# Performance work log

Measured on AMD Instinct MI355X. Metric: run time of the kernel, lower is better.

## Reference

```python
import jax, jax.numpy as jnp
import numpy as np

EPS = 1e-06        # normalize eps and log eps (module's self.eps)
PDIST_EPS = 1e-06  # torch.nn.PairwiseDistance default eps: ||x1 - x2 + eps||_2

A, C, F = 4096, 8, 64


def setup_inputs() -> dict:
    key = jax.random.key(0)
    x = jax.random.normal(key, (A, C, F), dtype=jnp.float32)
    return {"x": x}


def reference(x) -> jnp.ndarray:
    a = x.shape[0]
    c = x.shape[1]
    # F.normalize(p=2, dim=-1, eps=EPS): x / max(||x||_2, eps)
    nrm = jnp.linalg.norm(x, axis=-1, keepdims=True)
    xn = x / jnp.maximum(nrm, EPS)
    # pairwise cosine similarity per group: [C, A, A]
    sim = jnp.einsum('acf,bcf->cab', xn, xn)
    # mask self-similarity on the diagonal with -1
    diag = jnp.eye(a, dtype=bool)[None, :, :]
    sim = jnp.where(diag, -1.0, sim)
    # nearest neighbor per (c, a): argmax over b -> [C, A] -> [A, C]
    idx = jnp.argmax(sim, axis=-1).T
    # gather matched embeddings: x_match[a, c, f] = xn[idx[a, c], c, f]
    x_match = xn[idx, jnp.arange(c)[None, :], :]
    # PairwiseDistance(p=2, eps=1e-6): ||x - x_match + eps||_2 over last dim
    min_dist = jnp.linalg.norm(xn - x_match + PDIST_EPS, axis=-1)
    loss = -jnp.mean(jnp.log(min_dist + EPS))
    return loss
```

## Files before the change

kernel.cpp:

```cpp
#include <hip/hip_runtime.h>
#include <math.h>

#define AN 4096
#define CN 8
#define FN 64
#define ACN (AN*CN)

typedef __attribute__((ext_vector_type(8))) short bf16x8;
typedef __attribute__((ext_vector_type(4))) float f32x4;

__device__ inline unsigned short f2bf(float f) {
    unsigned u = __float_as_uint(f);
    unsigned r = ((u >> 16) & 1) + 0x7FFFu;
    return (unsigned short)((u + r) >> 16);
}

__global__ __launch_bounds__(256) void k1_normalize(const float* __restrict__ x,
                                                    float* __restrict__ xn,
                                                    unsigned short* __restrict__ xnb)
{
    int tid  = threadIdx.x;
    int grp  = tid >> 4;
    int slot = tid & 15;
    int V = blockIdx.x * 16 + grp;
    const float4 v = *(const float4*)(x + (size_t)V * FN + slot * 4);
    float ss = v.x*v.x + v.y*v.y + v.z*v.z + v.w*v.w;
    ss += __shfl_xor(ss, 1);
    ss += __shfl_xor(ss, 2);
    ss += __shfl_xor(ss, 4);
    ss += __shfl_xor(ss, 8);
    float sc = 1.0f / fmaxf(sqrtf(ss), 1e-6f);
    float4 o; o.x = v.x*sc; o.y = v.y*sc; o.z = v.z*sc; o.w = v.w*sc;
    *(float4*)(xn + (size_t)V * FN + slot * 4) = o;
    int a = V >> 3, c = V & 7;
    ushort4 ob;
    ob.x = f2bf(o.x); ob.y = f2bf(o.y); ob.z = f2bf(o.z); ob.w = f2bf(o.w);
    *(ushort4*)(xnb + ((size_t)c * AN + a) * FN + slot * 4) = ob;
}

__global__ __launch_bounds__(256, 2) void k2_argmax(const unsigned short* __restrict__ xnb,
                                                    unsigned int* __restrict__ pP)
{
    __shared__ uint4 lds4[3 * 1024];

    int blk  = blockIdx.x;
    int half = blk & 1;
    int rt   = (blk >> 1) & 31;
    int c    = blk >> 6;
    int a0   = rt * 128;
    int b0base = half * 2048;

    const uint4* __restrict__ Xc4 = (const uint4*)(xnb + (size_t)c * AN * FN);

    int tid  = threadIdx.x;
    int lane = tid & 63;
    int w    = tid >> 6;
    int wr   = w >> 1;
    int wc   = w & 1;
    int l15  = lane & 15;
    int quad = lane >> 4;

    int srow   = tid >> 3;
    int schunk = tid & 7;

    #pragma unroll
    for (int s = 0; s < 4; ++s) {
        int r = srow + 32 * s;
        lds4[r * 8 + (schunk ^ (r & 7))] = Xc4[(size_t)(a0 + r) * 8 + schunk];
    }
    #pragma unroll
    for (int s = 0; s < 4; ++s) {
        int r = srow + 32 * s;
        lds4[1024 + r * 8 + (schunk ^ (r & 7))] = Xc4[(size_t)(b0base + r) * 8 + schunk];
    }
    __syncthreads();

    bf16x8 afr[4][2];
    #pragma unroll
    for (int mi = 0; mi < 4; ++mi)
        #pragma unroll
        for (int ks = 0; ks < 2; ++ks) {
            int r  = wr * 64 + mi * 16 + l15;
            int ch = (ks * 4 + quad) ^ (r & 7);
            afr[mi][ks] = ((const bf16x8*)lds4)[r * 8 + ch];
        }

    float bestp[16];
    #pragma unroll
    for (int i = 0; i < 16; ++i) bestp[i] = 0.0f;

    const f32x4 two = {2.0f, 2.0f, 2.0f, 2.0f};

    for (int it = 0; it < 16; ++it) {
        int cur = it & 1;
        uint4 gv[4];
        if (it < 15) {
            int g0 = b0base + (it + 1) * 128;
            #pragma unroll
            for (int s = 0; s < 4; ++s)
                gv[s] = Xc4[(size_t)(g0 + srow + 32 * s) * 8 + schunk];
        }

        f32x4 acc[4][4];
        const bf16x8* bt = (const bf16x8*)(lds4 + 1024 + cur * 1024);
        #pragma unroll
        for (int ks = 0; ks < 2; ++ks) {
            #pragma unroll
            for (int ni = 0; ni < 4; ++ni) {
                int r  = wc * 64 + ni * 16 + l15;
                int ch = (ks * 4 + quad) ^ (r & 7);
                bf16x8 bfr = bt[r * 8 + ch];
                #pragma unroll
                for (int mi = 0; mi < 4; ++mi)
                    acc[mi][ni] = __builtin_amdgcn_mfma_f32_16x16x32_bf16(
                        afr[mi][ks], bfr, (ks == 0) ? two : acc[mi][ni], 0, 0, 0);
            }
        }

        int colblk = b0base + it * 128 + wc * 64;
        #pragma unroll
        for (int ni = 0; ni < 4; ++ni) {
            int cfrag = colblk + ni * 16;
            unsigned code = (unsigned)(cfrag + l15);
            #pragma unroll
            for (int mi = 0; mi < 4; ++mi) {
                int rfrag = a0 + wr * 64 + mi * 16;
                bool dg = (rfrag == cfrag);
                #pragma unroll
                for (int r = 0; r < 4; ++r) {
                    unsigned pb = (__float_as_uint(acc[mi][ni][r]) & 0xFFFFF000u) | code;
                    if (dg && (l15 == quad * 4 + r)) pb = 0u;
                    int bi = mi * 4 + r;
                    bestp[bi] = fmaxf(bestp[bi], __uint_as_float(pb));
                }
            }
        }

        if (it < 15) {
            #pragma unroll
            for (int s = 0; s < 4; ++s) {
                int r = srow + 32 * s;
                lds4[1024 + (cur ^ 1) * 1024 + r * 8 + (schunk ^ (r & 7))] = gv[s];
            }
        }
        __syncthreads();
    }

    #pragma unroll
    for (int i = 0; i < 16; ++i) {
        float v = bestp[i];
        v = fmaxf(v, __shfl_xor(v, 1));
        v = fmaxf(v, __shfl_xor(v, 2));
        v = fmaxf(v, __shfl_xor(v, 4));
        v = fmaxf(v, __shfl_xor(v, 8));
        bestp[i] = v;
    }
    __syncthreads();
    float* red = (float*)lds4;
    if (l15 == 0) {
        #pragma unroll
        for (int mi = 0; mi < 4; ++mi)
            #pragma unroll
            for (int r = 0; r < 4; ++r)
                red[w * 64 + mi * 16 + quad * 4 + r] = bestp[mi * 4 + r];
    }
    __syncthreads();
    if (tid < 128) {
        int wr2 = tid >> 6, r64 = tid & 63;
        float p = fmaxf(red[(2 * wr2) * 64 + r64], red[(2 * wr2 + 1) * 64 + r64]);
        int a = a0 + tid;
        pP[(size_t)half * ACN + (size_t)a * CN + c] = __float_as_uint(p);
    }
}

__global__ __launch_bounds__(256) void k3_dist(const float* __restrict__ xn,
                                               const unsigned int* __restrict__ pP,
                                               float* __restrict__ partials)
{
    int id = blockIdx.x * 256 + threadIdx.x;
    float p0 = __uint_as_float(pP[id]);
    float p1 = __uint_as_float(pP[ACN + id]);
    unsigned pm = __float_as_uint(fmaxf(p0, p1));
    int m = (int)(pm & 0xFFFu);
    int c = id & 7;
    const float* xa = xn + (size_t)id * FN;
    const float* xb = xn + ((size_t)m * CN + c) * FN;
    float ss = 0.0f;
    #pragma unroll
    for (int q = 0; q < 16; ++q) {
        float4 va = *(const float4*)(xa + 4 * q);
        float4 vb = *(const float4*)(xb + 4 * q);
        float d0 = va.x - vb.x + 1e-6f;
        float d1 = va.y - vb.y + 1e-6f;
        float d2 = va.z - vb.z + 1e-6f;
        float d3 = va.w - vb.w + 1e-6f;
        ss += d0*d0 + d1*d1 + d2*d2 + d3*d3;
    }
    float val = logf(sqrtf(ss) + 1e-6f);

    float t = val;
    #pragma unroll
    for (int off = 32; off > 0; off >>= 1) t += __shfl_down(t, off);
    __shared__ float ws4[4];
    if ((threadIdx.x & 63) == 0) ws4[threadIdx.x >> 6] = t;
    __syncthreads();
    if (threadIdx.x == 0)
        partials[blockIdx.x] = ws4[0] + ws4[1] + ws4[2] + ws4[3];
}

__global__ __launch_bounds__(64) void k4_final(const float* __restrict__ partials,
                                               float* __restrict__ out)
{
    int t = threadIdx.x;
    float v = partials[t] + partials[t + 64];
    #pragma unroll
    for (int off = 32; off > 0; off >>= 1) v += __shfl_down(v, off);
    if (t == 0) out[0] = -v / (float)ACN;
}

extern "C" void kernel_launch(void* const* d_in, const int* in_sizes, int n_in,
                              void* d_out, int out_size, void* d_ws, size_t ws_size,
                              hipStream_t stream)
{
    const float* x = (const float*)d_in[0];
    float* ws = (float*)d_ws;
    float* xn = ws;
    unsigned short* xnb = (unsigned short*)(xn + (size_t)AN * CN * FN);
    unsigned int* pP = (unsigned int*)(xnb + (size_t)AN * CN * FN);
    float* partials = (float*)(pP + 2 * ACN);

    k1_normalize<<<2048, 256, 0, stream>>>(x, xn, xnb);
    k2_argmax  <<<512, 256, 0, stream>>>(xnb, pP);
    k3_dist    <<<128, 256, 0, stream>>>(xn, pP, partials);
    k4_final   <<<1, 64, 0, stream>>>(partials, (float*)d_out);
}
```

Baseline: 94.67 us.

## Fuse all stages into one cooperative kernel with grid syncs; drop fp32 xn buffer

Merges normalize, argmax, distance and final reduction into a single cooperative kernel separated by grid-wide syncs, which removes three launch gaps. The fp32 normalized copy is no longer written. Instead, per-row inverse norms are stored, and the distance stage rescales the raw input on the fly, cutting global write and read traffic. Grid syncs add barrier cost and need all 512 blocks co-resident, so a fallback path of separate kernels remains.

```diff
diff --git a/kernel.cpp b/kernel.cpp
--- a/kernel.cpp
+++ b/kernel.cpp
@@ -1,5 +1,8 @@
 #include <hip/hip_runtime.h>
+#include <hip/hip_cooperative_groups.h>
 #include <math.h>
+
+namespace cg = cooperative_groups;
 
 #define AN 4096
 #define CN 8
@@ -15,35 +18,36 @@
     return (unsigned short)((u + r) >> 16);
 }
 
-__global__ __launch_bounds__(256) void k1_normalize(const float* __restrict__ x,
-                                                    float* __restrict__ xn,
-                                                    unsigned short* __restrict__ xnb)
-{
-    int tid  = threadIdx.x;
+__device__ inline void phase1_normalize(const float* __restrict__ x,
+                                        unsigned short* __restrict__ xnb,
+                                        float* __restrict__ inv,
+                                        int blk, int tid)
+{
     int grp  = tid >> 4;
     int slot = tid & 15;
-    int V = blockIdx.x * 16 + grp;
-    const float4 v = *(const float4*)(x + (size_t)V * FN + slot * 4);
-    float ss = v.x*v.x + v.y*v.y + v.z*v.z + v.w*v.w;
-    ss += __shfl_xor(ss, 1);
-    ss += __shfl_xor(ss, 2);
-    ss += __shfl_xor(ss, 4);
-    ss += __shfl_xor(ss, 8);
-    float sc = 1.0f / fmaxf(sqrtf(ss), 1e-6f);
-    float4 o; o.x = v.x*sc; o.y = v.y*sc; o.z = v.z*sc; o.w = v.w*sc;
-    *(float4*)(xn + (size_t)V * FN + slot * 4) = o;
-    int a = V >> 3, c = V & 7;
-    ushort4 ob;
-    ob.x = f2bf(o.x); ob.y = f2bf(o.y); ob.z = f2bf(o.z); ob.w = f2bf(o.w);
-    *(ushort4*)(xnb + ((size_t)c * AN + a) * FN + slot * 4) = ob;
-}
-
-__global__ __launch_bounds__(256, 2) void k2_argmax(const unsigned short* __restrict__ xnb,
-                                                    unsigned int* __restrict__ pP)
-{
-    __shared__ uint4 lds4[3 * 1024];
-
-    int blk  = blockIdx.x;
+    #pragma unroll
+    for (int s = 0; s < 4; ++s) {
+        int V = blk * 64 + s * 16 + grp;
+        const float4 v = *(const float4*)(x + (size_t)V * FN + slot * 4);
+        float ss = v.x*v.x + v.y*v.y + v.z*v.z + v.w*v.w;
+        ss += __shfl_xor(ss, 1);
+        ss += __shfl_xor(ss, 2);
+        ss += __shfl_xor(ss, 4);
+        ss += __shfl_xor(ss, 8);
+        float sc = 1.0f / fmaxf(sqrtf(ss), 1e-6f);
+        int a = V >> 3, c = V & 7;
+        ushort4 ob;
+        ob.x = f2bf(v.x * sc); ob.y = f2bf(v.y * sc);
+        ob.z = f2bf(v.z * sc); ob.w = f2bf(v.w * sc);
+        *(ushort4*)(xnb + ((size_t)c * AN + a) * FN + slot * 4) = ob;
+        if (slot == 0) inv[V] = sc;
+    }
+}
+
+__device__ inline void phase2_argmax(const unsigned short* __restrict__ xnb,
+                                     unsigned int* __restrict__ pP,
+                                     uint4* lds4, int blk, int tid)
+{
     int half = blk & 1;
     int rt   = (blk >> 1) & 31;
     int c    = blk >> 6;
@@ -52,7 +56,6 @@
 
     const uint4* __restrict__ Xc4 = (const uint4*)(xnb + (size_t)c * AN * FN);
 
-    int tid  = threadIdx.x;
     int lane = tid & 63;
     int w    = tid >> 6;
     int wr   = w >> 1;
@@ -125,14 +128,18 @@
             #pragma unroll
             for (int mi = 0; mi < 4; ++mi) {
                 int rfrag = a0 + wr * 64 + mi * 16;
-                bool dg = (rfrag == cfrag);
+                unsigned pbv[4];
                 #pragma unroll
-                for (int r = 0; r < 4; ++r) {
-                    unsigned pb = (__float_as_uint(acc[mi][ni][r]) & 0xFFFFF000u) | code;
-                    if (dg && (l15 == quad * 4 + r)) pb = 0u;
-                    int bi = mi * 4 + r;
-                    bestp[bi] = fmaxf(bestp[bi], __uint_as_float(pb));
+                for (int r = 0; r < 4; ++r)
+                    pbv[r] = (__float_as_uint(acc[mi][ni][r]) & 0xFFFFF000u) | code;
+                if (rfrag == cfrag) {
+                    #pragma unroll
+                    for (int r = 0; r < 4; ++r)
+                        if (l15 == quad * 4 + r) pbv[r] = 0u;
                 }
+                #pragma unroll
+                for (int r = 0; r < 4; ++r)
+                    bestp[mi * 4 + r] = fmaxf(bestp[mi * 4 + r], __uint_as_float(pbv[r]));
             }
         }
 
@@ -173,43 +180,95 @@
     }
 }
 
-__global__ __launch_bounds__(256) void k3_dist(const float* __restrict__ xn,
-                                               const unsigned int* __restrict__ pP,
-                                               float* __restrict__ partials)
-{
-    int id = blockIdx.x * 256 + threadIdx.x;
+__device__ inline void phase3_dist(const float* __restrict__ x,
+                                   const float* __restrict__ inv,
+                                   const unsigned int* __restrict__ pP,
+                                   float* __restrict__ partials,
+                                   int blk, int tid, float* sharedf)
+{
+    if (blk >= 128) return;
+    int id = blk * 256 + tid;
     float p0 = __uint_as_float(pP[id]);
     float p1 = __uint_as_float(pP[ACN + id]);
     unsigned pm = __float_as_uint(fmaxf(p0, p1));
     int m = (int)(pm & 0xFFFu);
     int c = id & 7;
-    const float* xa = xn + (size_t)id * FN;
-    const float* xb = xn + ((size_t)m * CN + c) * FN;
+    int idb = m * CN + c;
+    float sa = inv[id];
+    float sb = inv[idb];
+    const float* xa = x + (size_t)id  * FN;
+    const float* xb = x + (size_t)idb * FN;
     float ss = 0.0f;
     #pragma unroll
     for (int q = 0; q < 16; ++q) {
         float4 va = *(const float4*)(xa + 4 * q);
         float4 vb = *(const float4*)(xb + 4 * q);
-        float d0 = va.x - vb.x + 1e-6f;
-        float d1 = va.y - vb.y + 1e-6f;
-        float d2 = va.z - vb.z + 1e-6f;
-        float d3 = va.w - vb.w + 1e-6f;
+        float d0 = va.x * sa - vb.x * sb + 1e-6f;
+        float d1 = va.y * sa - vb.y * sb + 1e-6f;
+        float d2 = va.z * sa - vb.z * sb + 1e-6f;
+        float d3 = va.w * sa - vb.w * sb + 1e-6f;
         ss += d0*d0 + d1*d1 + d2*d2 + d3*d3;
     }
-    float val = logf(sqrtf(ss) + 1e-6f);
-
-    float t = val;
+    float t = logf(sqrtf(ss) + 1e-6f);
     #pragma unroll
     for (int off = 32; off > 0; off >>= 1) t += __shfl_down(t, off);
-    __shared__ float ws4[4];
-    if ((threadIdx.x & 63) == 0) ws4[threadIdx.x >> 6] = t;
+    if ((tid & 63) == 0) sharedf[tid >> 6] = t;
     __syncthreads();
-    if (threadIdx.x == 0)
-        partials[blockIdx.x] = ws4[0] + ws4[1] + ws4[2] + ws4[3];
-}
-
-__global__ __launch_bounds__(64) void k4_final(const float* __restrict__ partials,
-                                               float* __restrict__ out)
+    if (tid == 0)
+        partials[blk] = sharedf[0] + sharedf[1] + sharedf[2] + sharedf[3];
+}
+
+__global__ __launch_bounds__(256, 2) void k_fused(const float* __restrict__ x,
+                                                  unsigned short* __restrict__ xnb,
+                                                  float* __restrict__ inv,
+                                                  unsigned int* __restrict__ pP,
+                                                  float* __restrict__ partials,
+                                                  float* __restrict__ out)
+{
+    __shared__ uint4 lds4[3 * 1024];
+    int tid = threadIdx.x;
+    int blk = blockIdx.x;
+    cg::grid_group g = cg::this_grid();
+
+    phase1_normalize(x, xnb, inv, blk, tid);
+    g.sync();
+    phase2_argmax(xnb, pP, lds4, blk, tid);
+    g.sync();
+    phase3_dist(x, inv, pP, partials, blk, tid, (float*)lds4);
+    g.sync();
+    if (blk == 0 && tid < 64) {
+        float v = partials[tid] + partials[tid + 64];
+        #pragma unroll
+        for (int off = 32; off > 0; off >>= 1) v += __shfl_down(v, off);
+        if (tid == 0) out[0] = -v / (float)ACN;
+    }
+}
+
+__global__ __launch_bounds__(256) void k1s(const float* __restrict__ x,
+                                           unsigned short* __restrict__ xnb,
+                                           float* __restrict__ inv)
+{
+    phase1_normalize(x, xnb, inv, blockIdx.x, threadIdx.x);
+}
+
+__global__ __launch_bounds__(256, 2) void k2s(const unsigned short* __restrict__ xnb,
+                                              unsigned int* __restrict__ pP)
+{
+    __shared__ uint4 lds4[3 * 1024];
+    phase2_argmax(xnb, pP, lds4, blockIdx.x, threadIdx.x);
+}
+
+__global__ __launch_bounds__(256) void k3s(const float* __restrict__ x,
+                                           const float* __restrict__ inv,
+                                           const unsigned int* __restrict__ pP,
+                                           float* __restrict__ partials)
+{
+    __shared__ float sharedf[4];
+    phase3_dist(x, inv, pP, partials, blockIdx.x, threadIdx.x, sharedf);
+}
+
+__global__ __launch_bounds__(64) void k4s(const float* __restrict__ partials,
+                                          float* __restrict__ out)
 {
     int t = threadIdx.x;
     float v = partials[t] + partials[t + 64];
@@ -223,14 +282,27 @@
                               hipStream_t stream)
 {
     const float* x = (const float*)d_in[0];
-    float* ws = (float*)d_ws;
-    float* xn = ws;
-    unsigned short* xnb = (unsigned short*)(xn + (size_t)AN * CN * FN);
-    unsigned int* pP = (unsigned int*)(xnb + (size_t)AN * CN * FN);
+    unsigned short* xnb = (unsigned short*)d_ws;
+    float* inv = (float*)(xnb + (size_t)AN * CN * FN);
+    unsigned int* pP = (unsigned int*)(inv + ACN);
     float* partials = (float*)(pP + 2 * ACN);
-
-    k1_normalize<<<2048, 256, 0, stream>>>(x, xn, xnb);
-    k2_argmax  <<<512, 256, 0, stream>>>(xnb, pP);
-    k3_dist    <<<128, 256, 0, stream>>>(xn, pP, partials);
-    k4_final   <<<1, 64, 0, stream>>>(partials, (float*)d_out);
-}
+    float* outf = (float*)d_out;
+
+    void* args[6];
+    args[0] = (void*)&x;
+    args[1] = (void*)&xnb;
+    args[2] = (void*)&inv;
+    args[3] = (void*)&pP;
+    args[4] = (void*)&partials;
+    args[5] = (void*)&outf;
+
+    hipError_t err = hipLaunchCooperativeKernel((const void*)k_fused,
+                                                dim3(512), dim3(256),
+                                                args, 0, stream);
+    if (err != hipSuccess) {
+        k1s<<<512, 256, 0, stream>>>(x, xnb, inv);
+        k2s<<<512, 256, 0, stream>>>(xnb, pP);
+        k3s<<<128, 256, 0, stream>>>(x, inv, pP, partials);
+        k4s<<<1, 64, 0, stream>>>(partials, outf);
+    }
+}
```

Result: slower. 274.0 us (+189.4%).

## Drop fp32 normalized copy, store inverse norms, restructure argmax epilogue

Applied to the files above, without the earlier changes.

The normalize kernel no longer writes an fp32 normalized copy. It writes only the bf16 transposed copy plus one inverse norm per vector, and each thread now handles four vectors with a quarter as many blocks. The distance kernel reads the raw input and rescales it by the stored inverse norms, which removes an 8 MB write and its later read. The argmax epilogue is reordered to take the max over four candidates before merging into the running best, which shortens the dependency chain. Rounding may differ slightly because the scaling now happens inside the distance computation.

```diff
diff --git a/kernel.cpp b/kernel.cpp
--- a/kernel.cpp
+++ b/kernel.cpp
@@ -16,26 +16,29 @@
 }
 
 __global__ __launch_bounds__(256) void k1_normalize(const float* __restrict__ x,
-                                                    float* __restrict__ xn,
-                                                    unsigned short* __restrict__ xnb)
+                                                    unsigned short* __restrict__ xnb,
+                                                    float* __restrict__ inv)
 {
     int tid  = threadIdx.x;
     int grp  = tid >> 4;
     int slot = tid & 15;
-    int V = blockIdx.x * 16 + grp;
-    const float4 v = *(const float4*)(x + (size_t)V * FN + slot * 4);
-    float ss = v.x*v.x + v.y*v.y + v.z*v.z + v.w*v.w;
-    ss += __shfl_xor(ss, 1);
-    ss += __shfl_xor(ss, 2);
-    ss += __shfl_xor(ss, 4);
-    ss += __shfl_xor(ss, 8);
-    float sc = 1.0f / fmaxf(sqrtf(ss), 1e-6f);
-    float4 o; o.x = v.x*sc; o.y = v.y*sc; o.z = v.z*sc; o.w = v.w*sc;
-    *(float4*)(xn + (size_t)V * FN + slot * 4) = o;
-    int a = V >> 3, c = V & 7;
-    ushort4 ob;
-    ob.x = f2bf(o.x); ob.y = f2bf(o.y); ob.z = f2bf(o.z); ob.w = f2bf(o.w);
-    *(ushort4*)(xnb + ((size_t)c * AN + a) * FN + slot * 4) = ob;
+    #pragma unroll
+    for (int s = 0; s < 4; ++s) {
+        int V = blockIdx.x * 64 + s * 16 + grp;
+        const float4 v = *(const float4*)(x + (size_t)V * FN + slot * 4);
+        float ss = v.x*v.x + v.y*v.y + v.z*v.z + v.w*v.w;
+        ss += __shfl_xor(ss, 1);
+        ss += __shfl_xor(ss, 2);
+        ss += __shfl_xor(ss, 4);
+        ss += __shfl_xor(ss, 8);
+        float sc = 1.0f / fmaxf(sqrtf(ss), 1e-6f);
+        int a = V >> 3, c = V & 7;
+        ushort4 ob;
+        ob.x = f2bf(v.x * sc); ob.y = f2bf(v.y * sc);
+        ob.z = f2bf(v.z * sc); ob.w = f2bf(v.w * sc);
+        *(ushort4*)(xnb + ((size_t)c * AN + a) * FN + slot * 4) = ob;
+        if (slot == 0) inv[V] = sc;
+    }
 }
 
 __global__ __launch_bounds__(256, 2) void k2_argmax(const unsigned short* __restrict__ xnb,
@@ -118,21 +121,28 @@
         }
 
         int colblk = b0base + it * 128 + wc * 64;
-        #pragma unroll
-        for (int ni = 0; ni < 4; ++ni) {
-            int cfrag = colblk + ni * 16;
-            unsigned code = (unsigned)(cfrag + l15);
-            #pragma unroll
-            for (int mi = 0; mi < 4; ++mi) {
-                int rfrag = a0 + wr * 64 + mi * 16;
-                bool dg = (rfrag == cfrag);
+        int codebase = colblk + l15;
+        #pragma unroll
+        for (int mi = 0; mi < 4; ++mi) {
+            int rfrag = a0 + wr * 64 + mi * 16;
+            #pragma unroll
+            for (int r = 0; r < 4; ++r) {
+                float cand[4];
                 #pragma unroll
-                for (int r = 0; r < 4; ++r) {
-                    unsigned pb = (__float_as_uint(acc[mi][ni][r]) & 0xFFFFF000u) | code;
-                    if (dg && (l15 == quad * 4 + r)) pb = 0u;
-                    int bi = mi * 4 + r;
-                    bestp[bi] = fmaxf(bestp[bi], __uint_as_float(pb));
+                for (int ni = 0; ni < 4; ++ni) {
+                    unsigned pb = (__float_as_uint(acc[mi][ni][r]) & 0xFFFFF000u)
+                                | (unsigned)(codebase + ni * 16);
+                    cand[ni] = __uint_as_float(pb);
                 }
+                #pragma unroll
+                for (int ni = 0; ni < 4; ++ni) {
+                    if (rfrag == colblk + ni * 16) {
+                        if (l15 == quad * 4 + r) cand[ni] = 0.0f;
+                    }
+                }
+                int bi = mi * 4 + r;
+                bestp[bi] = fmaxf(fmaxf(fmaxf(fmaxf(cand[0], cand[1]), cand[2]),
+                                        cand[3]), bestp[bi]);
             }
         }
 
@@ -173,27 +183,32 @@
     }
 }
 
-__global__ __launch_bounds__(256) void k3_dist(const float* __restrict__ xn,
+__global__ __launch_bounds__(256) void k3_dist(const float* __restrict__ x,
+                                               const float* __restrict__ inv,
                                                const unsigned int* __restrict__ pP,
                                                float* __restrict__ partials)
 {
-    int id = blockIdx.x * 256 + threadIdx.x;
+    int tid = threadIdx.x;
+    int id = blockIdx.x * 256 + tid;
     float p0 = __uint_as_float(pP[id]);
     float p1 = __uint_as_float(pP[ACN + id]);
     unsigned pm = __float_as_uint(fmaxf(p0, p1));
     int m = (int)(pm & 0xFFFu);
     int c = id & 7;
-    const float* xa = xn + (size_t)id * FN;
-    const float* xb = xn + ((size_t)m * CN + c) * FN;
+    int idb = m * CN + c;
+    float sa = inv[id];
+    float sb = inv[idb];
+    const float* xa = x + (size_t)id  * FN;
+    const float* xb = x + (size_t)idb * FN;
     float ss = 0.0f;
     #pragma unroll
     for (int q = 0; q < 16; ++q) {
         float4 va = *(const float4*)(xa + 4 * q);
         float4 vb = *(const float4*)(xb + 4 * q);
-        float d0 = va.x - vb.x + 1e-6f;
-        float d1 = va.y - vb.y + 1e-6f;
-        float d2 = va.z - vb.z + 1e-6f;
-        float d3 = va.w - vb.w + 1e-6f;
+        float d0 = va.x * sa - vb.x * sb + 1e-6f;
+        float d1 = va.y * sa - vb.y * sb + 1e-6f;
+        float d2 = va.z * sa - vb.z * sb + 1e-6f;
+        float d3 = va.w * sa - vb.w * sb + 1e-6f;
         ss += d0*d0 + d1*d1 + d2*d2 + d3*d3;
     }
     float val = logf(sqrtf(ss) + 1e-6f);
@@ -202,9 +217,9 @@
     #pragma unroll
     for (int off = 32; off > 0; off >>= 1) t += __shfl_down(t, off);
     __shared__ float ws4[4];
-    if ((threadIdx.x & 63) == 0) ws4[threadIdx.x >> 6] = t;
-    __syncthreads();
-    if (threadIdx.x == 0)
+    if ((tid & 63) == 0) ws4[tid >> 6] = t;
+    __syncthreads();
+    if (tid == 0)
         partials[blockIdx.x] = ws4[0] + ws4[1] + ws4[2] + ws4[3];
 }
 
@@ -223,14 +238,13 @@
                               hipStream_t stream)
 {
     const float* x = (const float*)d_in[0];
-    float* ws = (float*)d_ws;
-    float* xn = ws;
-    unsigned short* xnb = (unsigned short*)(xn + (size_t)AN * CN * FN);
-    unsigned int* pP = (unsigned int*)(xnb + (size_t)AN * CN * FN);
+    unsigned short* xnb = (unsigned short*)d_ws;
+    float* inv = (float*)(xnb + (size_t)AN * CN * FN);
+    unsigned int* pP = (unsigned int*)(inv + ACN);
     float* partials = (float*)(pP + 2 * ACN);
 
-    k1_normalize<<<2048, 256, 0, stream>>>(x, xn, xnb);
+    k1_normalize<<<512, 256, 0, stream>>>(x, xnb, inv);
     k2_argmax  <<<512, 256, 0, stream>>>(xnb, pP);
-    k3_dist    <<<128, 256, 0, stream>>>(xn, pP, partials);
+    k3_dist    <<<128, 256, 0, stream>>>(x, inv, pP, partials);
     k4_final   <<<1, 64, 0, stream>>>(partials, (float*)d_out);
 }
```

After: 91.92 us. 1.03x faster.
